# Kernel tuning notes

Measured on AMD Instinct MI355X. Metric: run time of the kernel, lower is better.

The kernel has to match this reference:

```python
import jax, jax.numpy as jnp
import numpy as np

E, ME, K, N, G = 8, 1024, 2048, 2048, 128  # experts, tokens/expert, in, out, group size
M = E * ME

def setup_inputs() -> dict:
    key = jax.random.key(0)
    k1, k2, k3, k4, k5 = jax.random.split(key, 5)
    # int8 activations (values in [-128,127]), int4 weights (values in [-8,7])
    a_q = jax.random.randint(k1, (M, K), -128, 128, dtype=jnp.int32)
    w_q = jax.random.randint(k2, (E, N, K), -8, 8, dtype=jnp.int32)
    # quantization scales
    per_tok_scales = jax.random.uniform(k3, (M,), minval=0.5, maxval=1.5) / 127.0
    per_chan_scales = jax.random.uniform(k4, (E, N), minval=0.5, maxval=1.5) / 7.0
    w_group_scales = jax.random.uniform(k5, (E, N, K // G), minval=0.5, maxval=1.5)
    return {"a_q": a_q, "w_q": w_q, "per_tok_scales": per_tok_scales,
            "per_chan_scales": per_chan_scales, "w_group_scales": w_group_scales}

def reference(a_q, w_q, per_tok_scales, per_chan_scales, w_group_scales):
    # Grouped W4A8 GEMM: tokens are contiguous per expert (equal-size groups),
    # so reshape to [E, ME, K] and batch the per-expert GEMMs.
    a = a_q.reshape(E, ME, K).astype(jnp.float32)
    # dequantize int4 weights with per-(n, k-group) scales broadcast over the group
    w = w_q.astype(jnp.float32) * jnp.repeat(w_group_scales, G, axis=2)  # [E,N,K]
    raw = jnp.einsum('emk,enk->emn', a, w)  # [E,ME,N]
    out = raw * per_tok_scales.reshape(E, ME, 1) * per_chan_scales[:, None, :]
    return out.reshape(M, N)
```

## Files before the change

kernel.cpp:

```cpp
#include <hip/hip_runtime.h>
#include <hip/hip_bf16.h>
#include <cstdint>
#include <cstddef>

#define NE 8
#define MEt 1024
#define KD 2048
#define ND 2048
#define NG 16

#define BM 256
#define BN 256
#define BK 128
#define NKT (KD / BK)
#define TILE_B (BM * BK)

typedef int   i32x4  __attribute__((ext_vector_type(4)));
typedef int   i32x16 __attribute__((ext_vector_type(16)));
typedef float f32x16 __attribute__((ext_vector_type(16)));

#define A_ROWS (NE * MEt)
#define W_ROWS (NE * ND)
#define A_BYTES ((size_t)A_ROWS * KD)
#define PP_ROWS 8

__device__ __forceinline__ unsigned pack4(int x0, int x1, int x2, int x3) {
    return (unsigned)(x0 & 0xFF) | ((unsigned)(x1 & 0xFF) << 8) |
           ((unsigned)(x2 & 0xFF) << 16) | ((unsigned)x3 << 24);
}

__device__ __forceinline__ void gl_lds16(const void* g, void* l) {
    __builtin_amdgcn_global_load_lds(
        (const __attribute__((address_space(1))) void*)g,
        (__attribute__((address_space(3))) void*)l, 16, 0, 0);
}

__global__ __launch_bounds__(512)
void w4a8_prepack(const int* __restrict__ a_q, const int* __restrict__ w_q,
                  unsigned char* __restrict__ a8, unsigned char* __restrict__ w8)
{
    __shared__ __align__(16) int lbuf[PP_ROWS * KD];

    const int b   = blockIdx.x;
    const int tid = threadIdx.x;
    const int* src;
    unsigned char* dst;
    int rowbase;
    if (b < A_ROWS / PP_ROWS) { src = a_q; dst = a8; rowbase = b * PP_ROWS; }
    else                      { src = w_q; dst = w8; rowbase = (b - A_ROWS / PP_ROWS) * PP_ROWS; }

    const int wv   = tid >> 6;
    const int lane = tid & 63;

    const unsigned char* sb = (const unsigned char*)(src + (size_t)rowbase * KD);
    unsigned char* lb = (unsigned char*)lbuf;
#pragma unroll
    for (int i = 0; i < 8; ++i) {
        int chunk = wv * 8 + i;
        gl_lds16(sb + (size_t)chunk * 1024 + lane * 16, lb + chunk * 1024);
    }
    __syncthreads();

    const int kc = lane >> 3;
    const int rr = lane & 7;
    const int p  = rowbase >> 8;
    const int r0 = rowbase & 255;
#pragma unroll
    for (int j = 0; j < 2; ++j) {
        int kt = j * 8 + wv;
        const int* lp = lbuf + rr * KD + kt * BK + kc * 16;
        i32x4 v0 = *(const i32x4*)(lp);
        i32x4 v1 = *(const i32x4*)(lp + 4);
        i32x4 v2 = *(const i32x4*)(lp + 8);
        i32x4 v3 = *(const i32x4*)(lp + 12);
        i32x4 pk;
        pk[0] = (int)pack4(v0[0], v0[1], v0[2], v0[3]);
        pk[1] = (int)pack4(v1[0], v1[1], v1[2], v1[3]);
        pk[2] = (int)pack4(v2[0], v2[1], v2[2], v2[3]);
        pk[3] = (int)pack4(v3[0], v3[1], v3[2], v3[3]);
        unsigned char* dp = dst + ((size_t)(p * NKT + kt) * TILE_B)
                                + (size_t)(kc * 4096 + (r0 + rr) * 16);
        *(i32x4*)dp = pk;
    }
}

__device__ __forceinline__ void stage_tile(unsigned char* lds, const unsigned char* gtile,
                                           int wv, int lane) {
#pragma unroll
    for (int i = 0; i < 4; ++i) {
        int chunk = wv * 4 + i;
        gl_lds16(gtile + chunk * 1024 + lane * 16, lds + chunk * 1024);
    }
}

__global__ __launch_bounds__(512, 2)
void w4a8_gemm_pp(const unsigned char* __restrict__ a8,
                  const unsigned char* __restrict__ w8,
                  const float* __restrict__ per_tok,
                  const float* __restrict__ per_chan,
                  const float* __restrict__ wgs,
                  float* __restrict__ out)
{
    __shared__ __align__(16) unsigned char As[2][TILE_B];
    __shared__ __align__(16) unsigned char Bs[2][TILE_B];
    __shared__ float scs[NG][BN];

    int bid = blockIdx.x;
    int b2  = (bid & 7) * 32 + (bid >> 3);
    const int e  = b2 >> 5;
    const int tm = (b2 >> 3) & 3;
    const int tn = b2 & 7;

    const int tid  = threadIdx.x;
    const int lane = tid & 63;
    const int wv   = tid >> 6;
    const int wm   = wv >> 2;
    const int wn   = wv & 3;
    const int lcol = lane & 31;
    const int lhi  = lane >> 5;

    const unsigned char* Ag = a8 + (size_t)((e * 4 + tm) * NKT) * TILE_B;
    const unsigned char* Wg = w8 + (size_t)((e * 8 + tn) * NKT) * TILE_B;

    f32x16 facc[4][2] = {};
    const i32x16 z16 = {};

    stage_tile(As[0], Ag, wv, lane);
    stage_tile(Bs[0], Wg, wv, lane);
#pragma unroll
    for (int i = 0; i < 8; ++i) {
        int idx = tid + i * 512;
        int g = idx >> 8, n = idx & 255;
        scs[g][n] = wgs[((size_t)e * ND + tn * BN + n) * NG + g];
    }
    __syncthreads();

    int c = 0;
    for (int kt = 0; kt < NKT; ++kt) {
        if (kt + 1 < NKT) {
            stage_tile(As[c ^ 1], Ag + (kt + 1) * TILE_B, wv, lane);
            stage_tile(Bs[c ^ 1], Wg + (kt + 1) * TILE_B, wv, lane);
        }
        const unsigned char* Ac = As[c];
        const unsigned char* Bc = Bs[c];

        float sc0 = scs[kt][wn * 64 +  0 + lcol];
        float sc1 = scs[kt][wn * 64 + 32 + lcol];

        i32x4 bfr[2][4];
#pragma unroll
        for (int ni = 0; ni < 2; ++ni)
#pragma unroll
            for (int ks = 0; ks < 4; ++ks) {
                int kch = ks * 2 + lhi;
                bfr[ni][ks] = *(const i32x4*)&Bc[kch * (256 * 16) + (wn * 64 + ni * 32 + lcol) * 16];
            }

#pragma unroll
        for (int mi = 0; mi < 4; ++mi) {
            i32x4 afr[4];
#pragma unroll
            for (int ks = 0; ks < 4; ++ks) {
                int kch = ks * 2 + lhi;
                afr[ks] = *(const i32x4*)&Ac[kch * (256 * 16) + (wm * 128 + mi * 32 + lcol) * 16];
            }
            i32x16 acc0, acc1;
            acc0 = __builtin_amdgcn_mfma_i32_32x32x32_i8(afr[0], bfr[0][0], z16, 0, 0, 0);
            acc1 = __builtin_amdgcn_mfma_i32_32x32x32_i8(afr[0], bfr[1][0], z16, 0, 0, 0);
            acc0 = __builtin_amdgcn_mfma_i32_32x32x32_i8(afr[1], bfr[0][1], acc0, 0, 0, 0);
            acc1 = __builtin_amdgcn_mfma_i32_32x32x32_i8(afr[1], bfr[1][1], acc1, 0, 0, 0);
            acc0 = __builtin_amdgcn_mfma_i32_32x32x32_i8(afr[2], bfr[0][2], acc0, 0, 0, 0);
            acc1 = __builtin_amdgcn_mfma_i32_32x32x32_i8(afr[2], bfr[1][2], acc1, 0, 0, 0);
            acc0 = __builtin_amdgcn_mfma_i32_32x32x32_i8(afr[3], bfr[0][3], acc0, 0, 0, 0);
            acc1 = __builtin_amdgcn_mfma_i32_32x32x32_i8(afr[3], bfr[1][3], acc1, 0, 0, 0);
#pragma unroll
            for (int i = 0; i < 16; ++i) {
                facc[mi][0][i] += (float)acc0[i] * sc0;
                facc[mi][1][i] += (float)acc1[i] * sc1;
            }
        }
        __syncthreads();
        c ^= 1;
    }

    const float* ptok  = per_tok  + e * MEt + tm * BM;
    const float* pchan = per_chan + (size_t)e * ND + tn * BN;
    float* og = out + (size_t)(e * MEt + tm * BM) * ND + tn * BN;

#pragma unroll
    for (int mi = 0; mi < 4; ++mi) {
        int mb = wm * 128 + mi * 32;
#pragma unroll
        for (int ni = 0; ni < 2; ++ni) {
            int nn = wn * 64 + ni * 32 + lcol;
            float pc = pchan[nn];
#pragma unroll
            for (int rg = 0; rg < 16; ++rg) {
                int mr = mb + (rg & 3) + 8 * (rg >> 2) + 4 * lhi;
                float pt = ptok[mr];
                og[(size_t)mr * ND + nn] = facc[mi][ni][rg] * pt * pc;
            }
        }
    }
}

extern "C" void kernel_launch(void* const* d_in, const int* in_sizes, int n_in,
                              void* d_out, int out_size, void* d_ws, size_t ws_size,
                              hipStream_t stream) {
    const int*   a_q = (const int*)d_in[0];
    const int*   w_q = (const int*)d_in[1];
    const float* pt  = (const float*)d_in[2];
    const float* pc  = (const float*)d_in[3];
    const float* wg  = (const float*)d_in[4];
    float* out = (float*)d_out;

    unsigned char* a8 = (unsigned char*)d_ws;
    unsigned char* w8 = a8 + A_BYTES;

    w4a8_prepack<<<dim3((A_ROWS + W_ROWS) / PP_ROWS), dim3(512), 0, stream>>>(a_q, w_q, a8, w8);
    w4a8_gemm_pp<<<dim3(256), dim3(512), 0, stream>>>(a8, w8, pt, pc, wg, out);
}
```

Baseline: 105.4 us.

## Make prepack persistent with double-buffered LDS staging and XOR swizzle

Replaces the one-block-per-8-rows prepack launch with 256 persistent blocks that each walk 12 row groups. The next group's global-to-LDS load is double-buffered and overlapped with packing the current group. An XOR swizzle on the LDS addresses is meant to avoid bank conflicts on the column-strided reads. This adds manual waitcnt and barrier handling, and each block now needs 128KB of LDS, which limits it to one block per CU.

```diff
diff --git a/kernel.cpp b/kernel.cpp
--- a/kernel.cpp
+++ b/kernel.cpp
@@ -22,7 +22,8 @@
 #define A_ROWS (NE * MEt)
 #define W_ROWS (NE * ND)
 #define A_BYTES ((size_t)A_ROWS * KD)
-#define PP_ROWS 8
+#define PP_BLOCKS 256
+#define PP_ITERS  12
 
 __device__ __forceinline__ unsigned pack4(int x0, int x1, int x2, int x3) {
     return (unsigned)(x0 & 0xFF) | ((unsigned)(x1 & 0xFF) << 8) |
@@ -39,48 +40,71 @@
 void w4a8_prepack(const int* __restrict__ a_q, const int* __restrict__ w_q,
                   unsigned char* __restrict__ a8, unsigned char* __restrict__ w8)
 {
-    __shared__ __align__(16) int lbuf[PP_ROWS * KD];
-
-    const int b   = blockIdx.x;
-    const int tid = threadIdx.x;
-    const int* src;
-    unsigned char* dst;
-    int rowbase;
-    if (b < A_ROWS / PP_ROWS) { src = a_q; dst = a8; rowbase = b * PP_ROWS; }
-    else                      { src = w_q; dst = w8; rowbase = (b - A_ROWS / PP_ROWS) * PP_ROWS; }
-
+    __shared__ __align__(16) unsigned char lbuf[2][65536];
+
+    const int b    = blockIdx.x;
+    const int tid  = threadIdx.x;
     const int wv   = tid >> 6;
     const int lane = tid & 63;
-
-    const unsigned char* sb = (const unsigned char*)(src + (size_t)rowbase * KD);
-    unsigned char* lb = (unsigned char*)lbuf;
-#pragma unroll
-    for (int i = 0; i < 8; ++i) {
-        int chunk = wv * 8 + i;
-        gl_lds16(sb + (size_t)chunk * 1024 + lane * 16, lb + chunk * 1024);
-    }
-    __syncthreads();
-
-    const int kc = lane >> 3;
-    const int rr = lane & 7;
-    const int p  = rowbase >> 8;
-    const int r0 = rowbase & 255;
-#pragma unroll
-    for (int j = 0; j < 2; ++j) {
-        int kt = j * 8 + wv;
-        const int* lp = lbuf + rr * KD + kt * BK + kc * 16;
-        i32x4 v0 = *(const i32x4*)(lp);
-        i32x4 v1 = *(const i32x4*)(lp + 4);
-        i32x4 v2 = *(const i32x4*)(lp + 8);
-        i32x4 v3 = *(const i32x4*)(lp + 12);
-        i32x4 pk;
-        pk[0] = (int)pack4(v0[0], v0[1], v0[2], v0[3]);
-        pk[1] = (int)pack4(v1[0], v1[1], v1[2], v1[3]);
-        pk[2] = (int)pack4(v2[0], v2[1], v2[2], v2[3]);
-        pk[3] = (int)pack4(v3[0], v3[1], v3[2], v3[3]);
-        unsigned char* dp = dst + ((size_t)(p * NKT + kt) * TILE_B)
-                                + (size_t)(kc * 4096 + (r0 + rr) * 16);
-        *(i32x4*)dp = pk;
+    const int kc   = lane >> 3;
+    const int rr   = lane & 7;
+
+    auto issue = [&](int it, int s) {
+        int R = (b * PP_ITERS + it) * 8;
+        const unsigned char* srcb;
+        if (R < A_ROWS) srcb = (const unsigned char*)a_q + (size_t)(R + wv) * 8192;
+        else            srcb = (const unsigned char*)w_q + (size_t)(R - A_ROWS + wv) * 8192;
+        unsigned char* lb = &lbuf[s][wv * 8192];
+#pragma unroll
+        for (int i = 0; i < 8; ++i) {
+            int off = (i * 1024 + lane * 16) ^ (wv << 4);
+            gl_lds16(srcb + off, lb + i * 1024);
+        }
+    };
+
+    issue(0, 0);
+
+    for (int it = 0; it < PP_ITERS; ++it) {
+        if (it + 1 < PP_ITERS) {
+            issue(it + 1, (it + 1) & 1);
+            asm volatile("s_waitcnt vmcnt(8)" ::: "memory");
+        } else {
+            asm volatile("s_waitcnt vmcnt(0)" ::: "memory");
+        }
+        __builtin_amdgcn_sched_barrier(0);
+        __builtin_amdgcn_s_barrier();
+
+        const unsigned char* lb = lbuf[it & 1];
+        i32x4 v[2][4];
+#pragma unroll
+        for (int j = 0; j < 2; ++j) {
+            int kt = j * 8 + wv;
+#pragma unroll
+            for (int q = 0; q < 4; ++q) {
+                int addr = (rr * 8192 + kt * 512 + kc * 64 + q * 16) ^ (rr << 4);
+                v[j][q] = *(const i32x4*)&lb[addr];
+            }
+        }
+        asm volatile("s_waitcnt lgkmcnt(0)" ::: "memory");
+        __builtin_amdgcn_sched_barrier(0);
+        __builtin_amdgcn_s_barrier();
+
+        int R = (b * PP_ITERS + it) * 8;
+        unsigned char* dstb; int p, r0;
+        if (R < A_ROWS) { dstb = a8; p = R >> 8; r0 = R & 255; }
+        else { int Rw = R - A_ROWS; dstb = w8; p = Rw >> 8; r0 = Rw & 255; }
+#pragma unroll
+        for (int j = 0; j < 2; ++j) {
+            int kt = j * 8 + wv;
+            i32x4 pk;
+            pk[0] = (int)pack4(v[j][0][0], v[j][0][1], v[j][0][2], v[j][0][3]);
+            pk[1] = (int)pack4(v[j][1][0], v[j][1][1], v[j][1][2], v[j][1][3]);
+            pk[2] = (int)pack4(v[j][2][0], v[j][2][1], v[j][2][2], v[j][2][3]);
+            pk[3] = (int)pack4(v[j][3][0], v[j][3][1], v[j][3][2], v[j][3][3]);
+            unsigned char* dp = dstb + (size_t)(p * NKT + kt) * TILE_B
+                                     + (size_t)(kc * 4096 + (r0 + rr) * 16);
+            *(i32x4*)dp = pk;
+        }
     }
 }
 
@@ -217,6 +241,6 @@
     unsigned char* a8 = (unsigned char*)d_ws;
     unsigned char* w8 = a8 + A_BYTES;
 
-    w4a8_prepack<<<dim3((A_ROWS + W_ROWS) / PP_ROWS), dim3(512), 0, stream>>>(a_q, w_q, a8, w8);
+    w4a8_prepack<<<dim3(PP_BLOCKS), dim3(512), 0, stream>>>(a_q, w_q, a8, w8);
     w4a8_gemm_pp<<<dim3(256), dim3(512), 0, stream>>>(a8, w8, pt, pc, wg, out);
 }
```

Result: slower. 107.9 us (+2.4%).
